# Kernel optimization log

Hardware: AMD Instinct MI355X
Metric: run time of the kernel (lower is better)

## Reference

```python
import jax, jax.numpy as jnp
import numpy as np

S, B, V, E, H, L, HM = 256, 16, 20000, 512, 256, 2, 128  # seq, batch, vocab, emb, hidden, layers, mlp hidden
THRESH = 0.5


def setup_inputs() -> dict:
    key = jax.random.key(0)
    ks = jax.random.split(key, 8)
    sc = 0.05
    concepts = jax.random.randint(ks[0], (S, B), 0, V)
    concepts_lengths = jnp.full((B,), S, dtype=jnp.int32)  # full-length sequences
    emb = jax.random.normal(ks[1], (V, E), jnp.float32) * sc
    # stacked PyTorch-style LSTM weights: [layer, direction(0=fwd,1=bwd), 4H, in]
    w_ih = jax.random.normal(ks[2], (L, 2, 4 * H, E), jnp.float32) * sc
    w_hh = jax.random.normal(ks[3], (L, 2, 4 * H, H), jnp.float32) * sc
    b = jax.random.normal(ks[4], (L, 2, 4 * H), jnp.float32) * sc  # b_ih + b_hh combined
    Ua = jax.random.normal(ks[5], (HM, 2 * H), jnp.float32) * sc
    Wa = jax.random.normal(ks[6], (HM, 2 * H), jnp.float32) * sc
    va = jax.random.normal(ks[7], (1, HM), jnp.float32) * sc
    return dict(concepts=concepts, concepts_lengths=concepts_lengths, emb=emb,
                w_ih=w_ih, w_hh=w_hh, b=b, Ua=Ua, Wa=Wa, va=va)


def _lstm_dir(x, wi, wh, bb, reverse):
    # x: [S, B, in]; PyTorch gate order i, f, g, o
    h0 = jnp.zeros((x.shape[1], H), x.dtype)

    def step(carry, xt):
        h, c = carry
        g = xt @ wi.T + h @ wh.T + bb  # [B, 4H]
        i, f, gg, o = jnp.split(g, 4, axis=-1)
        c = jax.nn.sigmoid(f) * c + jax.nn.sigmoid(i) * jnp.tanh(gg)
        h = jax.nn.sigmoid(o) * jnp.tanh(c)
        return (h, c), h

    _, hs = jax.lax.scan(step, (h0, h0), x, reverse=reverse)
    return hs  # [S, B, H]


def reference(concepts, concepts_lengths, emb, w_ih, w_hh, b, Ua, Wa, va):
    x = emb[concepts]  # [S, B, E]
    for l in range(L):  # fixed small layer count
        f = _lstm_dir(x, w_ih[l, 0], w_hh[l, 0], b[l, 0], False)
        r = _lstm_dir(x, w_ih[l, 1], w_hh[l, 1], b[l, 1], True)
        x = jnp.concatenate([f, r], axis=-1)  # [S, B, 2H]
    enc = x.transpose(1, 0, 2)  # [B, S, 2H]
    p = enc @ Ua.T  # [B, S, HM]  Ua(parent)
    c = enc @ Wa.T  # [B, S, HM]  Wa(child)
    # fused pairwise: va(tanh(Ua(p_i) + Wa(c_j))) -> [B, S, S]
    scores = jnp.einsum('bijh,h->bij', jnp.tanh(p[:, :, None, :] + c[:, None, :, :]), va[0])
    predictions = (jax.nn.sigmoid(scores) >= THRESH).astype(jnp.int32)
    return scores, predictions
```

## Files before the change

### kernel.cpp

```cpp
#include <hip/hip_runtime.h>


#define S_    256
#define B_    16
#define E_    512
#define H_    256
#define HM_   128
#define M_    4096

typedef __attribute__((ext_vector_type(8))) short short8;
typedef __attribute__((ext_vector_type(4))) float f32x4;
union u32x4s8 { unsigned int u[4]; uint4 u4; short8 v; };

__device__ __forceinline__ float sigm(float x) { return 1.f / (1.f + __expf(-x)); }
__device__ __forceinline__ float tanh_fast(float x) {
  x = fminf(fmaxf(x, -15.f), 15.f);
  float e = __expf(2.f * x);
  return (e - 1.f) / (e + 1.f);
}
__device__ __forceinline__ unsigned short f2bf(float f) {
  unsigned u = __float_as_uint(f);
  u += 0x7FFFu + ((u >> 16) & 1u);
  return (unsigned short)(u >> 16);
}
__device__ __forceinline__ float bf2f(unsigned short s) {
  return __uint_as_float(((unsigned)s) << 16);
}
__device__ __forceinline__ unsigned int packsplit(float f) {
  unsigned short m = f2bf(f);
  unsigned short r = f2bf(f - bf2f(m));
  return (unsigned)m | ((unsigned)r << 16);
}

__global__ void k_gather_pk(const int* __restrict__ concepts, const float* __restrict__ emb,
                            unsigned int* __restrict__ Xpk) {
  int m = blockIdx.x;
  int tok = concepts[m];
  const float4* src = reinterpret_cast<const float4*>(emb + (size_t)tok * E_);
  uint4* dst = reinterpret_cast<uint4*>(Xpk + (size_t)m * E_);
  for (int i = threadIdx.x; i < E_ / 4; i += blockDim.x) {
    float4 v = src[i];
    uint4 o;
    o.x = packsplit(v.x); o.y = packsplit(v.y); o.z = packsplit(v.z); o.w = packsplit(v.w);
    dst[i] = o;
  }
}

__global__ void k_pack(const float* __restrict__ in, unsigned int* __restrict__ out, int n4) {
  int i = blockIdx.x * blockDim.x + threadIdx.x;
  if (i < n4) {
    float4 v = reinterpret_cast<const float4*>(in)[i];
    uint4 o;
    o.x = packsplit(v.x); o.y = packsplit(v.y); o.z = packsplit(v.z); o.w = packsplit(v.w);
    reinterpret_cast<uint4*>(out)[i] = o;
  }
}

__global__ __launch_bounds__(256) void k_gemm_pk(const unsigned int* __restrict__ Apk,
                                                 const unsigned int* __restrict__ Wpk,
                                                 const float* __restrict__ bias,
                                                 float* __restrict__ C, int N, int K) {
  __shared__ unsigned int As[128][36];
  __shared__ unsigned int Ws2[128][36];
  const int bm = blockIdx.x * 128, bn = blockIdx.y * 128;
  const int tid = threadIdx.x;
  const int wave = tid >> 6, lane = tid & 63;
  const int wm = (wave >> 1) << 6, wn = (wave & 1) << 6;
  const int l16 = lane & 15, quad = lane >> 4;
  const int r = tid >> 1, cb = (tid & 1) << 4;

  f32x4 acc[4][4];
#pragma unroll
  for (int i = 0; i < 4; ++i)
#pragma unroll
    for (int j = 0; j < 4; ++j) acc[i][j] = (f32x4){0.f, 0.f, 0.f, 0.f};

  for (int k0 = 0; k0 < K; k0 += 32) {
    const unsigned int* pa = Apk + (size_t)(bm + r) * K + k0 + cb;
    const unsigned int* pw = Wpk + (size_t)(bn + r) * K + k0 + cb;
    uint4 a0 = *(const uint4*)pa, a1 = *(const uint4*)(pa + 4),
          a2 = *(const uint4*)(pa + 8), a3 = *(const uint4*)(pa + 12);
    uint4 w0 = *(const uint4*)pw, w1 = *(const uint4*)(pw + 4),
          w2 = *(const uint4*)(pw + 8), w3 = *(const uint4*)(pw + 12);
    __syncthreads();
    *(uint4*)&As[r][cb] = a0;  *(uint4*)&As[r][cb + 4] = a1;
    *(uint4*)&As[r][cb + 8] = a2; *(uint4*)&As[r][cb + 12] = a3;
    *(uint4*)&Ws2[r][cb] = w0; *(uint4*)&Ws2[r][cb + 4] = w1;
    *(uint4*)&Ws2[r][cb + 8] = w2; *(uint4*)&Ws2[r][cb + 12] = w3;
    __syncthreads();

    short8 Amv[4], Arv[4], Bmv[4], Brv[4];
#pragma unroll
    for (int t = 0; t < 4; ++t) {
      const unsigned int* p = &As[wm + (t << 4) + l16][quad << 3];
      uint4 p0 = *(const uint4*)p, p1 = *(const uint4*)(p + 4);
      u32x4s8 m, rr;
      m.u[0] = __builtin_amdgcn_perm(p0.y, p0.x, 0x05040100u);
      rr.u[0] = __builtin_amdgcn_perm(p0.y, p0.x, 0x07060302u);
      m.u[1] = __builtin_amdgcn_perm(p0.w, p0.z, 0x05040100u);
      rr.u[1] = __builtin_amdgcn_perm(p0.w, p0.z, 0x07060302u);
      m.u[2] = __builtin_amdgcn_perm(p1.y, p1.x, 0x05040100u);
      rr.u[2] = __builtin_amdgcn_perm(p1.y, p1.x, 0x07060302u);
      m.u[3] = __builtin_amdgcn_perm(p1.w, p1.z, 0x05040100u);
      rr.u[3] = __builtin_amdgcn_perm(p1.w, p1.z, 0x07060302u);
      Amv[t] = m.v; Arv[t] = rr.v;
      const unsigned int* pb = &Ws2[wn + (t << 4) + l16][quad << 3];
      uint4 q0 = *(const uint4*)pb, q1 = *(const uint4*)(pb + 4);
      m.u[0] = __builtin_amdgcn_perm(q0.y, q0.x, 0x05040100u);
      rr.u[0] = __builtin_amdgcn_perm(q0.y, q0.x, 0x07060302u);
      m.u[1] = __builtin_amdgcn_perm(q0.w, q0.z, 0x05040100u);
      rr.u[1] = __builtin_amdgcn_perm(q0.w, q0.z, 0x07060302u);
      m.u[2] = __builtin_amdgcn_perm(q1.y, q1.x, 0x05040100u);
      rr.u[2] = __builtin_amdgcn_perm(q1.y, q1.x, 0x07060302u);
      m.u[3] = __builtin_amdgcn_perm(q1.w, q1.z, 0x05040100u);
      rr.u[3] = __builtin_amdgcn_perm(q1.w, q1.z, 0x07060302u);
      Bmv[t] = m.v; Brv[t] = rr.v;
    }
#pragma unroll
    for (int ti = 0; ti < 4; ++ti)
#pragma unroll
      for (int tj = 0; tj < 4; ++tj) {
        acc[ti][tj] = __builtin_amdgcn_mfma_f32_16x16x32_bf16(Amv[ti], Bmv[tj], acc[ti][tj], 0, 0, 0);
        acc[ti][tj] = __builtin_amdgcn_mfma_f32_16x16x32_bf16(Amv[ti], Brv[tj], acc[ti][tj], 0, 0, 0);
        acc[ti][tj] = __builtin_amdgcn_mfma_f32_16x16x32_bf16(Arv[ti], Bmv[tj], acc[ti][tj], 0, 0, 0);
      }
  }

  float bv[4];
#pragma unroll
  for (int tj = 0; tj < 4; ++tj)
    bv[tj] = bias ? bias[bn + wn + (tj << 4) + l16] : 0.f;
#pragma unroll
  for (int ti = 0; ti < 4; ++ti)
#pragma unroll
    for (int rr = 0; rr < 4; ++rr) {
      float* crow = C + (size_t)(bm + wm + (ti << 4) + (quad << 2) + rr) * N + bn + wn + l16;
      crow[0]  = acc[ti][0][rr] + bv[0];
      crow[16] = acc[ti][1][rr] + bv[1];
      crow[32] = acc[ti][2][rr] + bv[2];
      crow[48] = acc[ti][3][rr] + bv[3];
    }
}

__global__ __launch_bounds__(256) void k_gemm(const float* __restrict__ A,
                                              const float* __restrict__ W,
                                              const float* __restrict__ bias,
                                              float* __restrict__ C,
                                              int M, int N, int K) {
  __shared__ __align__(16) float As[16][132];
  __shared__ __align__(16) float Ws[16][132];
  const int bm = blockIdx.x * 128, bn = blockIdx.y * 128;
  const int tid = threadIdx.x;
  const int tm = (tid >> 4) * 8, tn = (tid & 15) * 8;
  float acc[8][8];
#pragma unroll
  for (int i = 0; i < 8; i++)
#pragma unroll
    for (int j = 0; j < 8; j++) acc[i][j] = 0.f;

  const int lr = tid >> 1, lk = (tid & 1) * 8;
  for (int k0 = 0; k0 < K; k0 += 16) {
    float4 a0 = *(const float4*)(A + (size_t)(bm + lr) * K + k0 + lk);
    float4 a1 = *(const float4*)(A + (size_t)(bm + lr) * K + k0 + lk + 4);
    float4 w0 = *(const float4*)(W + (size_t)(bn + lr) * K + k0 + lk);
    float4 w1 = *(const float4*)(W + (size_t)(bn + lr) * K + k0 + lk + 4);
    As[lk + 0][lr] = a0.x; As[lk + 1][lr] = a0.y; As[lk + 2][lr] = a0.z; As[lk + 3][lr] = a0.w;
    As[lk + 4][lr] = a1.x; As[lk + 5][lr] = a1.y; As[lk + 6][lr] = a1.z; As[lk + 7][lr] = a1.w;
    Ws[lk + 0][lr] = w0.x; Ws[lk + 1][lr] = w0.y; Ws[lk + 2][lr] = w0.z; Ws[lk + 3][lr] = w0.w;
    Ws[lk + 4][lr] = w1.x; Ws[lk + 5][lr] = w1.y; Ws[lk + 6][lr] = w1.z; Ws[lk + 7][lr] = w1.w;
    __syncthreads();
#pragma unroll
    for (int k = 0; k < 16; k++) {
      float4 av0 = *(const float4*)&As[k][tm];
      float4 av1 = *(const float4*)&As[k][tm + 4];
      float4 wv0 = *(const float4*)&Ws[k][tn];
      float4 wv1 = *(const float4*)&Ws[k][tn + 4];
      float a[8] = {av0.x, av0.y, av0.z, av0.w, av1.x, av1.y, av1.z, av1.w};
      float w[8] = {wv0.x, wv0.y, wv0.z, wv0.w, wv1.x, wv1.y, wv1.z, wv1.w};
#pragma unroll
      for (int i = 0; i < 8; i++)
#pragma unroll
        for (int j = 0; j < 8; j++) acc[i][j] += a[i] * w[j];
    }
    __syncthreads();
  }

  float bv[8];
#pragma unroll
  for (int j = 0; j < 8; j++) bv[j] = bias ? bias[bn + tn + j] : 0.f;
#pragma unroll
  for (int i = 0; i < 8; i++) {
    float4 v0 = make_float4(acc[i][0] + bv[0], acc[i][1] + bv[1], acc[i][2] + bv[2], acc[i][3] + bv[3]);
    float4 v1 = make_float4(acc[i][4] + bv[4], acc[i][5] + bv[5], acc[i][6] + bv[6], acc[i][7] + bv[7]);
    *(float4*)(C + (size_t)(bm + tm + i) * N + bn + tn) = v0;
    *(float4*)(C + (size_t)(bm + tm + i) * N + bn + tn + 4) = v1;
  }
}

__global__ __launch_bounds__(512) void k_lstm(const float* __restrict__ Gin,
                                              const float* __restrict__ whh,
                                              float* __restrict__ Houtf,
                                              unsigned int* __restrict__ Houtp,
                                              unsigned long long* __restrict__ Hbuf) {
  const int d = blockIdx.x >> 4;
  const int g = blockIdx.x & 15;
  const int tid = threadIdx.x;
  const int w8 = tid >> 6;
  const int lane = tid & 63;
  const int bcol = lane & 15;
  const int quad = lane >> 4;
  const int u_e = tid & 15;
  const int b_e = (tid >> 4) & 15;
  const int ws = (w8 + g) & 7;
  __shared__ unsigned int hL[16 * 260];
  __shared__ __align__(16) float Lg[4][16][24];

  unsigned int Am[8][4], Ar[8][4];
  if (w8 < 4) {
    const float* wrow = whh + (size_t)((d << 10) + (w8 << 8) + (g << 4) + bcol) * 256;
#pragma unroll
    for (int s = 0; s < 8; ++s) {
      float w[8];
      *(float4*)&w[0] = *(const float4*)(wrow + s * 32 + quad * 8);
      *(float4*)&w[4] = *(const float4*)(wrow + s * 32 + quad * 8 + 4);
#pragma unroll
      for (int j = 0; j < 4; ++j) {
        unsigned short m0 = f2bf(w[2 * j]), m1 = f2bf(w[2 * j + 1]);
        unsigned short r0 = f2bf(w[2 * j] - bf2f(m0));
        unsigned short r1 = f2bf(w[2 * j + 1] - bf2f(m1));
        Am[s][j] = (unsigned)m0 | ((unsigned)m1 << 16);
        Ar[s][j] = (unsigned)r0 | ((unsigned)r1 << 16);
      }
    }
  }

  float c_reg = 0.f;
  for (int it = 0; it < 256; ++it) {
    const int step = d ? (255 - it) : it;

    float gin[4];
    if (tid < 256) {
#pragma unroll
      for (int qq = 0; qq < 4; ++qq)
        gin[qq] = Gin[((size_t)((step << 4) + b_e) << 11) + (d << 10) + (qq << 8) + (g << 4) + u_e];
    }

    if (it > 0) {
      const unsigned long long* src = Hbuf + ((size_t)((d << 1) + ((it - 1) & 1)) << 12);
      const unsigned long long* p0 = src + (ws << 9) + lane;
      const unsigned int want = (unsigned int)it;
      unsigned long long v[8];
#pragma unroll
      for (int c = 0; c < 8; ++c)
        v[c] = __hip_atomic_load(p0 + (c << 6), __ATOMIC_RELAXED, __HIP_MEMORY_SCOPE_AGENT);
      for (;;) {
        unsigned int badm = 0;
#pragma unroll
        for (int c = 0; c < 8; ++c)
          badm |= ((unsigned int)(v[c] >> 32) != want) ? (1u << c) : 0u;
        if (__ballot(badm != 0) == 0ull) break;
#pragma unroll
        for (int c = 0; c < 8; ++c)
          if (badm & (1u << c))
            v[c] = __hip_atomic_load(p0 + (c << 6), __ATOMIC_RELAXED, __HIP_MEMORY_SCOPE_AGENT);
      }
#pragma unroll
      for (int c = 0; c < 8; ++c) {
        int e_b = (ws << 1) + (c >> 2);
        int e_k = ((c & 3) << 6) + lane;
        hL[e_b * 260 + e_k] = (unsigned int)v[c];
      }
    }
    __syncthreads();

    if (w8 < 4) {
      f32x4 acc0 = {0.f, 0.f, 0.f, 0.f}, acc1 = acc0, acc2 = acc0;
      if (it > 0) {
#pragma unroll
        for (int s = 0; s < 8; ++s) {
          const unsigned int* p = &hL[bcol * 260 + (s << 5) + (quad << 3)];
          uint4 p0v = *(const uint4*)p;
          uint4 p1v = *(const uint4*)(p + 4);
          u32x4s8 Bm, Br, Amu, Aru;
          Bm.u[0] = __builtin_amdgcn_perm(p0v.y, p0v.x, 0x05040100u);
          Br.u[0] = __builtin_amdgcn_perm(p0v.y, p0v.x, 0x07060302u);
          Bm.u[1] = __builtin_amdgcn_perm(p0v.w, p0v.z, 0x05040100u);
          Br.u[1] = __builtin_amdgcn_perm(p0v.w, p0v.z, 0x07060302u);
          Bm.u[2] = __builtin_amdgcn_perm(p1v.y, p1v.x, 0x05040100u);
          Br.u[2] = __builtin_amdgcn_perm(p1v.y, p1v.x, 0x07060302u);
          Bm.u[3] = __builtin_amdgcn_perm(p1v.w, p1v.z, 0x05040100u);
          Br.u[3] = __builtin_amdgcn_perm(p1v.w, p1v.z, 0x07060302u);
#pragma unroll
          for (int j = 0; j < 4; ++j) { Amu.u[j] = Am[s][j]; Aru.u[j] = Ar[s][j]; }
          acc0 = __builtin_amdgcn_mfma_f32_16x16x32_bf16(Amu.v, Bm.v, acc0, 0, 0, 0);
          acc1 = __builtin_amdgcn_mfma_f32_16x16x32_bf16(Amu.v, Br.v, acc1, 0, 0, 0);
          acc2 = __builtin_amdgcn_mfma_f32_16x16x32_bf16(Aru.v, Bm.v, acc2, 0, 0, 0);
        }
      }
      f32x4 t = acc0 + acc1 + acc2;
      *(float4*)&Lg[w8][bcol][quad << 2] = make_float4(t[0], t[1], t[2], t[3]);
    }
    __syncthreads();

    if (tid < 256) {
      float gi = Lg[0][b_e][u_e] + gin[0];
      float gf = Lg[1][b_e][u_e] + gin[1];
      float gg = Lg[2][b_e][u_e] + gin[2];
      float go = Lg[3][b_e][u_e] + gin[3];
      float ct = sigm(gf) * c_reg + sigm(gi) * tanh_fast(gg);
      c_reg = ct;
      float h = sigm(go) * tanh_fast(ct);
      unsigned short hm = f2bf(h);
      unsigned short hr = f2bf(h - bf2f(hm));
      unsigned int hpk = ((unsigned)hr << 16) | (unsigned)hm;
      unsigned long long hp = ((unsigned long long)(unsigned int)(it + 1) << 32) |
                              (unsigned long long)hpk;
      __hip_atomic_store(Hbuf + ((size_t)((d << 1) + (it & 1)) << 12) + (b_e << 8) + (g << 4) + u_e,
                         hp, __ATOMIC_RELAXED, __HIP_MEMORY_SCOPE_AGENT);
      size_t oidx = (size_t)((step << 4) + b_e) * 512 + (d << 8) + (g << 4) + u_e;
      Houtf[oidx] = h;
      Houtp[oidx] = hpk;
    }
  }
}

__global__ __launch_bounds__(256) void k_attn(const float* __restrict__ P,
                                              const float* __restrict__ Cc,
                                              const float* __restrict__ va,
                                              float* __restrict__ out) {
  const int b = blockIdx.x & 15, i = blockIdx.x >> 4;
  __shared__ float pv[128], vv[128];
  const int t = threadIdx.x;
  if (t < 128) {
    pv[t] = P[(size_t)((i << 4) + b) * 128 + t];
    vv[t] = va[t];
  }
  __syncthreads();
  const float4* c4 = reinterpret_cast<const float4*>(Cc + (size_t)((t << 4) + b) * 128);
  float acc = 0.f;
#pragma unroll 8
  for (int hh = 0; hh < 32; ++hh) {
    float4 cv = c4[hh];
    int h = hh << 2;
    acc += vv[h]     * tanh_fast(pv[h]     + cv.x);
    acc += vv[h + 1] * tanh_fast(pv[h + 1] + cv.y);
    acc += vv[h + 2] * tanh_fast(pv[h + 2] + cv.z);
    acc += vv[h + 3] * tanh_fast(pv[h + 3] + cv.w);
  }
  size_t o = ((size_t)b << 16) + ((size_t)i << 8) + (size_t)t;
  out[o] = acc;
  out[(1u << 20) + o] = (acc >= 0.f) ? 1.f : 0.f;
}

extern "C" void kernel_launch(void* const* d_in, const int* in_sizes, int n_in,
                              void* d_out, int out_size, void* d_ws, size_t ws_size,
                              hipStream_t stream) {
  const int*   concepts = (const int*)d_in[0];
  const float* emb  = (const float*)d_in[2];
  const float* w_ih = (const float*)d_in[3];
  const float* w_hh = (const float*)d_in[4];
  const float* bias = (const float*)d_in[5];
  const float* Ua   = (const float*)d_in[6];
  const float* Wa   = (const float*)d_in[7];
  const float* va   = (const float*)d_in[8];
  float* out = (float*)d_out;
  float* ws  = (float*)d_ws;

  constexpr size_t OFF_G   = 0;
  constexpr size_t OFF_PK  = OFF_G  + (size_t)M_ * 2048;
  constexpr size_t OFF_WPK = OFF_PK + (size_t)M_ * 512;
  constexpr size_t OFF_HF  = OFF_WPK + 2 * 2048 * 512;
  constexpr size_t OFF_P   = OFF_HF + (size_t)M_ * 512;
  constexpr size_t OFF_C   = OFF_P  + (size_t)M_ * HM_;
  constexpr size_t OFF_HB  = OFF_C  + (size_t)M_ * HM_;

  float* G  = ws + OFF_G;
  unsigned int* PK  = (unsigned int*)(ws + OFF_PK);
  unsigned int* WPK = (unsigned int*)(ws + OFF_WPK);
  float* HF = ws + OFF_HF;
  float* Pm = ws + OFF_P;
  float* Cm = ws + OFF_C;
  unsigned long long* Hb0 = (unsigned long long*)(ws + OFF_HB);
  unsigned long long* Hb1 = Hb0 + 2 * 2 * 4096;

  k_pack<<<(2 * 2048 * 512 / 4 + 255) / 256, 256, 0, stream>>>(w_ih, WPK, 2 * 2048 * 512 / 4);
  k_gather_pk<<<M_, 128, 0, stream>>>(concepts, emb, PK);

  k_gemm_pk<<<dim3(32, 16), 256, 0, stream>>>(PK, WPK, bias, G, 2048, 512);
  k_lstm<<<32, 512, 0, stream>>>(G, w_hh, HF, PK, Hb0);

  k_gemm_pk<<<dim3(32, 16), 256, 0, stream>>>(PK, WPK + (size_t)2048 * 512, bias + 2048,
                                              G, 2048, 512);
  k_lstm<<<32, 512, 0, stream>>>(G, w_hh + (size_t)2048 * 256, HF, PK, Hb1);

  k_gemm<<<dim3(32, 1), 256, 0, stream>>>(HF, Ua, nullptr, Pm, M_, HM_, 512);
  k_gemm<<<dim3(32, 1), 256, 0, stream>>>(HF, Wa, nullptr, Cm, M_, HM_, 512);

  k_attn<<<M_, 256, 0, stream>>>(Pm, Cm, va, out);
}
```

Baseline: 1.548 ms.

## Elect XCD-local LSTM teams and use cache-bypassing polling for hidden-state exchange

Launches 160 LSTM blocks. Each block reads its XCD id from a hardware register and counts arrivals per XCD with an atomic, so that two full 16-block teams sharing one XCD each take one direction and the extra blocks exit. The aim is to keep the per-step h exchange inside one XCD's L2 rather than crossing dies. Polling now uses inline sc0 loads and a duplicated plain store, with a fallback to the original atomic loop after repeated timeouts. The election and Hbuf buffers are zeroed in the gather kernel. The change adds launch overhead and relies on memory-coherence assumptions that may not hold, which could cause stale reads or hangs.

```diff
diff --git a/kernel.cpp b/kernel.cpp
--- a/kernel.cpp
+++ b/kernel.cpp
@@ -33,7 +33,13 @@
 }
 
 __global__ void k_gather_pk(const int* __restrict__ concepts, const float* __restrict__ emb,
-                            unsigned int* __restrict__ Xpk) {
+                            unsigned int* __restrict__ Xpk,
+                            unsigned long long* __restrict__ hbz,
+                            unsigned int* __restrict__ elect) {
+  if (blockIdx.x == 0)
+    for (int i = threadIdx.x; i < 192; i += blockDim.x) elect[i] = 0;
+  if (threadIdx.x < 8)
+    hbz[(size_t)blockIdx.x * 8 + threadIdx.x] = 0ull;
   int m = blockIdx.x;
   int tok = concepts[m];
   const float4* src = reinterpret_cast<const float4*>(emb + (size_t)tok * E_);
@@ -201,10 +207,51 @@
                                               const float* __restrict__ whh,
                                               float* __restrict__ Houtf,
                                               unsigned int* __restrict__ Houtp,
-                                              unsigned long long* __restrict__ Hbuf) {
-  const int d = blockIdx.x >> 4;
-  const int g = blockIdx.x & 15;
+                                              unsigned long long* __restrict__ Hbuf,
+                                              unsigned int* __restrict__ E) {
+  __shared__ int s_dg[2];
   const int tid = threadIdx.x;
+
+  if (tid == 0) {
+    int xcd = __builtin_amdgcn_s_getreg(20 | (0 << 6) | (31 << 11)) & 7;
+    unsigned rank = __hip_atomic_fetch_add(&E[xcd], 1u, __ATOMIC_RELAXED,
+                                           __HIP_MEMORY_SCOPE_AGENT);
+    unsigned team = rank >> 4, slot = rank & 15;
+    int role = -1;
+    if (team < 10) {
+      unsigned aidx = 10 + (unsigned)xcd * 10 + team;
+      if (slot == 15) {
+        unsigned c = __hip_atomic_fetch_add(&E[8], 1u, __ATOMIC_ACQ_REL,
+                                            __HIP_MEMORY_SCOPE_AGENT);
+        unsigned val = (c < 2) ? (c + 1) : 3u;
+        __hip_atomic_store(&E[aidx], val, __ATOMIC_RELEASE, __HIP_MEMORY_SCOPE_AGENT);
+        if (c < 2) {
+          __hip_atomic_fetch_add(&E[9], 1u, __ATOMIC_ACQ_REL, __HIP_MEMORY_SCOPE_AGENT);
+          role = (int)c;
+        }
+      } else {
+        for (;;) {
+          unsigned v = __hip_atomic_load(&E[aidx], __ATOMIC_ACQUIRE,
+                                         __HIP_MEMORY_SCOPE_AGENT);
+          if (v) { role = (v == 3) ? -1 : (int)v - 1; break; }
+          if (__hip_atomic_load(&E[9], __ATOMIC_ACQUIRE, __HIP_MEMORY_SCOPE_AGENT) >= 2) {
+            v = __hip_atomic_load(&E[aidx], __ATOMIC_ACQUIRE, __HIP_MEMORY_SCOPE_AGENT);
+            role = (v == 0 || v == 3) ? -1 : (int)v - 1;
+            break;
+          }
+          __builtin_amdgcn_s_sleep(8);
+        }
+      }
+      s_dg[0] = role; s_dg[1] = (int)slot;
+    } else {
+      s_dg[0] = -1; s_dg[1] = 0;
+    }
+  }
+  __syncthreads();
+  const int d = s_dg[0];
+  if (d < 0) return;
+  const int g = s_dg[1];
+
   const int w8 = tid >> 6;
   const int lane = tid & 63;
   const int bcol = lane & 15;
@@ -234,6 +281,8 @@
     }
   }
 
+  int faro = 0;
+  int fesc = 0;
   float c_reg = 0.f;
   for (int it = 0; it < 256; ++it) {
     const int step = d ? (255 - it) : it;
@@ -250,19 +299,50 @@
       const unsigned long long* p0 = src + (ws << 9) + lane;
       const unsigned int want = (unsigned int)it;
       unsigned long long v[8];
-#pragma unroll
-      for (int c = 0; c < 8; ++c)
-        v[c] = __hip_atomic_load(p0 + (c << 6), __ATOMIC_RELAXED, __HIP_MEMORY_SCOPE_AGENT);
-      for (;;) {
-        unsigned int badm = 0;
+      bool have = false;
+      if (!faro) {
+        int rounds = 0;
+        for (;;) {
+          asm volatile(
+            "global_load_dwordx2 %0, %8, off sc0\n\t"
+            "global_load_dwordx2 %1, %8, off offset:512 sc0\n\t"
+            "global_load_dwordx2 %2, %8, off offset:1024 sc0\n\t"
+            "global_load_dwordx2 %3, %8, off offset:1536 sc0\n\t"
+            "global_load_dwordx2 %4, %8, off offset:2048 sc0\n\t"
+            "global_load_dwordx2 %5, %8, off offset:2560 sc0\n\t"
+            "global_load_dwordx2 %6, %8, off offset:3072 sc0\n\t"
+            "global_load_dwordx2 %7, %8, off offset:3584 sc0\n\t"
+            "s_waitcnt vmcnt(0)"
+            : "=&v"(v[0]), "=&v"(v[1]), "=&v"(v[2]), "=&v"(v[3]),
+              "=&v"(v[4]), "=&v"(v[5]), "=&v"(v[6]), "=&v"(v[7])
+            : "v"(p0)
+            : "memory");
+          unsigned int badm = 0;
+#pragma unroll
+          for (int c = 0; c < 8; ++c)
+            badm |= ((unsigned int)(v[c] >> 32) != want) ? (1u << c) : 0u;
+          if (__ballot(badm != 0) == 0ull) { have = true; break; }
+          if (++rounds > 64) {
+            if (++fesc >= 8) faro = 1;
+            break;
+          }
+        }
+      }
+      if (!have) {
 #pragma unroll
         for (int c = 0; c < 8; ++c)
-          badm |= ((unsigned int)(v[c] >> 32) != want) ? (1u << c) : 0u;
-        if (__ballot(badm != 0) == 0ull) break;
-#pragma unroll
-        for (int c = 0; c < 8; ++c)
-          if (badm & (1u << c))
-            v[c] = __hip_atomic_load(p0 + (c << 6), __ATOMIC_RELAXED, __HIP_MEMORY_SCOPE_AGENT);
+          v[c] = __hip_atomic_load(p0 + (c << 6), __ATOMIC_RELAXED, __HIP_MEMORY_SCOPE_AGENT);
+        for (;;) {
+          unsigned int badm = 0;
+#pragma unroll
+          for (int c = 0; c < 8; ++c)
+            badm |= ((unsigned int)(v[c] >> 32) != want) ? (1u << c) : 0u;
+          if (__ballot(badm != 0) == 0ull) break;
+#pragma unroll
+          for (int c = 0; c < 8; ++c)
+            if (badm & (1u << c))
+              v[c] = __hip_atomic_load(p0 + (c << 6), __ATOMIC_RELAXED, __HIP_MEMORY_SCOPE_AGENT);
+        }
       }
 #pragma unroll
       for (int c = 0; c < 8; ++c) {
@@ -315,8 +395,11 @@
       unsigned int hpk = ((unsigned)hr << 16) | (unsigned)hm;
       unsigned long long hp = ((unsigned long long)(unsigned int)(it + 1) << 32) |
                               (unsigned long long)hpk;
-      __hip_atomic_store(Hbuf + ((size_t)((d << 1) + (it & 1)) << 12) + (b_e << 8) + (g << 4) + u_e,
-                         hp, __ATOMIC_RELAXED, __HIP_MEMORY_SCOPE_AGENT);
+      unsigned long long* dst = Hbuf + ((size_t)((d << 1) + (it & 1)) << 12) +
+                                (b_e << 8) + (g << 4) + u_e;
+      __hip_atomic_store(dst, hp, __ATOMIC_RELAXED, __HIP_MEMORY_SCOPE_AGENT);
+      asm volatile("global_store_dwordx2 %0, %1, off"
+                   :: "v"(dst), "v"(hp) : "memory");
       size_t oidx = (size_t)((step << 4) + b_e) * 512 + (d << 8) + (g << 4) + u_e;
       Houtf[oidx] = h;
       Houtp[oidx] = hpk;
@@ -382,16 +465,18 @@
   float* Cm = ws + OFF_C;
   unsigned long long* Hb0 = (unsigned long long*)(ws + OFF_HB);
   unsigned long long* Hb1 = Hb0 + 2 * 2 * 4096;
+  unsigned int* EL0 = (unsigned int*)Pm;
+  unsigned int* EL1 = EL0 + 96;
 
   k_pack<<<(2 * 2048 * 512 / 4 + 255) / 256, 256, 0, stream>>>(w_ih, WPK, 2 * 2048 * 512 / 4);
-  k_gather_pk<<<M_, 128, 0, stream>>>(concepts, emb, PK);
+  k_gather_pk<<<M_, 128, 0, stream>>>(concepts, emb, PK, Hb0, EL0);
 
   k_gemm_pk<<<dim3(32, 16), 256, 0, stream>>>(PK, WPK, bias, G, 2048, 512);
-  k_lstm<<<32, 512, 0, stream>>>(G, w_hh, HF, PK, Hb0);
+  k_lstm<<<160, 512, 0, stream>>>(G, w_hh, HF, PK, Hb0, EL0);
 
   k_gemm_pk<<<dim3(32, 16), 256, 0, stream>>>(PK, WPK + (size_t)2048 * 512, bias + 2048,
                                               G, 2048, 512);
-  k_lstm<<<32, 512, 0, stream>>>(G, w_hh + (size_t)2048 * 256, HF, PK, Hb1);
+  k_lstm<<<160, 512, 0, stream>>>(G, w_hh + (size_t)2048 * 256, HF, PK, Hb1, EL1);
 
   k_gemm<<<dim3(32, 1), 256, 0, stream>>>(HF, Ua, nullptr, Pm, M_, HM_, 512);
   k_gemm<<<dim3(32, 1), 256, 0, stream>>>(HF, Wa, nullptr, Cm, M_, HM_, 512);
```

Result: slower. 2.421 ms (+56.4%).
